# Optimization experiments

Measured on AMD Instinct MI355X. Metric: run time of the kernel, lower is better.

The kernel has to match this reference:

```python
import jax, jax.numpy as jnp
import numpy as np

B, H, W, C = 4, 448, 448, 3
P = 16
G = 28            # grid = H // P
T = G * G         # 784 patches
E = 768
HD = 3072
NH = 12
DH = E // NH
L = 6
LW = 9            # local_window


def _ln(x, g, b, eps=1e-5):
    m = x.mean(-1, keepdims=True)
    v = ((x - m) ** 2).mean(-1, keepdims=True)
    return (x - m) / jnp.sqrt(v + eps) * g + b


def _mask_bias():
    # torch bool attn_mask: True = disallowed. The module sets True for LOCAL
    # neighbors (|dr|<=lw//2 and |dc|<=lw//2), so local positions are MASKED OUT.
    idx = jnp.arange(T)
    r, c = idx // G, idx % G
    local = (jnp.abs(r[:, None] - r[None, :]) <= LW // 2) & \
            (jnp.abs(c[:, None] - c[None, :]) <= LW // 2)
    return jnp.where(local, -jnp.inf, 0.0).astype(jnp.float32)  # [T, T]


def _img_to_patch(x):
    # x: [B,H,W,C] -> [B,T,C*P*P], channel-major within a patch (matches torch code)
    x = x.transpose(0, 3, 1, 2)                       # [B,C,H,W]
    x = x.reshape(B, C, G, P, G, P)
    x = x.transpose(0, 2, 4, 1, 3, 5)                 # [B,G,G,C,P,P]
    return x.reshape(B, T, C * P * P)


def _forward(x, sxr_mean, sxr_std, input_w, input_b, pos_emb,
             ln1_w, ln1_b, in_w, in_b, out_w, out_b, ln2_w, ln2_b,
             w1, b1, w2, b2, head_ln_w, head_ln_b, head_w, head_b):
    h = _img_to_patch(x) @ input_w.T + input_b        # [B,T,E]
    h = (h.reshape(B, G, G, E) + pos_emb).reshape(B, T, E)
    bias = _mask_bias()

    def block(h, prm):
        l1w, l1b, iw, ib, ow, ob, l2w, l2b, W1, B1, W2, B2 = prm
        y = _ln(h, l1w, l1b)
        qkv = y @ iw.T + ib                           # [B,T,3E]
        q, k, v = jnp.split(qkv, 3, axis=-1)
        q = q.reshape(B, T, NH, DH)
        k = k.reshape(B, T, NH, DH)
        v = v.reshape(B, T, NH, DH)
        s = jnp.einsum('bqhd,bkhd->bhqk', q, k) / jnp.sqrt(jnp.float32(DH)) + bias
        a = jax.nn.softmax(s, axis=-1)
        o = jnp.einsum('bhqk,bkhd->bqhd', a, v).reshape(B, T, E)
        h = h + o @ ow.T + ob
        y2 = _ln(h, l2w, l2b)
        m = jax.nn.gelu(y2 @ W1.T + B1, approximate=False)  # torch nn.GELU default
        h = h + m @ W2.T + B2
        return h, None

    h, _ = jax.lax.scan(block, h, (ln1_w, ln1_b, in_w, in_b, out_w, out_b,
                                   ln2_w, ln2_b, w1, b1, w2, b2))

    logits = (_ln(h, head_ln_w, head_ln_b) @ head_w.T + head_b)[..., 0]  # [B,T]
    patch_flux = jnp.clip(10.0 ** (logits * sxr_std[0] + sxr_mean[0]) - 1e-8,
                          1e-15, 1.0)
    global_flux = jnp.maximum(patch_flux.sum(axis=1, keepdims=True), 1e-15)
    return global_flux, patch_flux


def setup_inputs() -> dict:
    key = jax.random.key(0)
    ks = iter(jax.random.split(key, 16))
    def p(shape, s=0.02):
        return jax.random.normal(next(ks), shape, jnp.float32) * s
    return dict(
        x=jax.random.normal(next(ks), (B, H, W, C), jnp.float32),
        sxr_mean=jnp.array([-6.0], jnp.float32),
        sxr_std=jnp.array([1.0], jnp.float32),
        input_w=p((E, C * P * P)), input_b=jnp.zeros(E, jnp.float32),
        pos_emb=p((1, G, G, E), 1.0),
        ln1_w=jnp.ones((L, E), jnp.float32), ln1_b=jnp.zeros((L, E), jnp.float32),
        in_w=p((L, 3 * E, E)), in_b=jnp.zeros((L, 3 * E), jnp.float32),
        out_w=p((L, E, E)), out_b=jnp.zeros((L, E), jnp.float32),
        ln2_w=jnp.ones((L, E), jnp.float32), ln2_b=jnp.zeros((L, E), jnp.float32),
        w1=p((L, HD, E)), b1=jnp.zeros((L, HD), jnp.float32),
        w2=p((L, E, HD)), b2=jnp.zeros((L, E), jnp.float32),
        head_ln_w=jnp.ones(E, jnp.float32), head_ln_b=jnp.zeros(E, jnp.float32),
        head_w=p((1, E)), head_b=jnp.zeros(1, jnp.float32),
    )


def reference(x, sxr_mean, sxr_std, input_w, input_b, pos_emb,
              ln1_w, ln1_b, in_w, in_b, out_w, out_b, ln2_w, ln2_b,
              w1, b1, w2, b2, head_ln_w, head_ln_b, head_w, head_b):
    return _forward(x, sxr_mean, sxr_std, input_w, input_b, pos_emb,
                    ln1_w, ln1_b, in_w, in_b, out_w, out_b, ln2_w, ln2_b,
                    w1, b1, w2, b2, head_ln_w, head_ln_b, head_w, head_b)
```

## Files before the change

### kernel.cpp

```cpp
#include <hip/hip_runtime.h>
#include <math.h>

#define BB 4
#define TT 784
#define GG 28
#define EE 768
#define HDIM 3072
#define NHEAD 12
#define NLAYER 6

typedef short bfrag __attribute__((ext_vector_type(8)));
typedef float ffrag __attribute__((ext_vector_type(4)));

__device__ __forceinline__ unsigned short f2b(float f) {
    union { float f; unsigned u; } v; v.f = f;
    unsigned r = v.u + 0x7FFF + ((v.u >> 16) & 1);
    return (unsigned short)(r >> 16);
}

#define GLOAD_LDS16(g, l)                                                          \
    __builtin_amdgcn_global_load_lds(                                              \
        (const __attribute__((address_space(1))) void*)(g),                        \
        (__attribute__((address_space(3))) void*)(l), 16, 0, 0)

__device__ __forceinline__ float block_reduce_sum256(float v, volatile float* sb) {
    #pragma unroll
    for (int m = 1; m < 64; m <<= 1) v += __shfl_xor(v, m, 64);
    int wave = threadIdx.x >> 6;
    if ((threadIdx.x & 63) == 0) sb[wave] = v;
    __syncthreads();
    return sb[0] + sb[1] + sb[2] + sb[3];
}

__global__ __launch_bounds__(256) void cast_kernel(const float* __restrict__ s,
                                                   unsigned short* __restrict__ d, int n4) {
    int i = blockIdx.x * 256 + threadIdx.x;
    if (i >= n4) return;
    float4 v = ((const float4*)s)[i];
    ushort4 o;
    o.x = f2b(v.x); o.y = f2b(v.y); o.z = f2b(v.z); o.w = f2b(v.w);
    ((ushort4*)d)[i] = o;
}

__global__ __launch_bounds__(256) void fused_cast_kernel(const float* __restrict__ iw,
                                                         const float* __restrict__ ow,
                                                         const float* __restrict__ W1,
                                                         const float* __restrict__ W2,
                                                         unsigned short* __restrict__ dq,
                                                         unsigned short* __restrict__ doo,
                                                         unsigned short* __restrict__ d1,
                                                         unsigned short* __restrict__ d2) {
    int i = blockIdx.x * 256 + threadIdx.x;
    const float* s; unsigned short* d; int k;
    if (i < 442368)            { s = iw;  d = dq;  k = i; }
    else if (i < 589824)       { s = ow;  d = doo; k = i - 442368; }
    else if (i < 1179648)      { s = W1;  d = d1;  k = i - 589824; }
    else if (i < 1769472)      { s = W2;  d = d2;  k = i - 1179648; }
    else return;
    float4 v = ((const float4*)s)[k];
    ushort4 o;
    o.x = f2b(v.x); o.y = f2b(v.y); o.z = f2b(v.z); o.w = f2b(v.w);
    ((ushort4*)d)[k] = o;
}

__global__ __launch_bounds__(256) void patchify_kernel(const float* __restrict__ x,
                                                       unsigned short* __restrict__ P) {
    int idx = blockIdx.x * blockDim.x + threadIdx.x;
    const int total = BB * TT * EE;
    if (idx >= total) return;
    int k = idx % EE;
    int t = (idx / EE) % TT;
    int b = idx / (EE * TT);
    int c = k >> 8;
    int rem = k & 255;
    int p1 = rem >> 4;
    int p2 = rem & 15;
    int g1 = t / GG, g2 = t % GG;
    int hh = g1 * 16 + p1, ww = g2 * 16 + p2;
    P[idx] = f2b(x[((b * 448 + hh) * 448 + ww) * 3 + c]);
}

__global__ __launch_bounds__(256) void posfill_kernel(float* __restrict__ h,
                                                      const float* __restrict__ pos) {
    int idx = blockIdx.x * blockDim.x + threadIdx.x;
    const int total = BB * TT * EE;
    if (idx >= total) return;
    h[idx] = pos[idx % (TT * EE)];
}

__global__ __launch_bounds__(256) void ln_kernel(const float* __restrict__ X,
                                                 const float* __restrict__ g,
                                                 const float* __restrict__ bt,
                                                 unsigned short* __restrict__ Yb,
                                                 float* Yf) {
    __shared__ float sb1[4];
    __shared__ float sb2[4];
    int row = blockIdx.x;
    int tid = threadIdx.x;
    const float* x = X + (size_t)row * EE;
    float v0 = x[tid], v1 = x[tid + 256], v2 = x[tid + 512];
    float s = block_reduce_sum256(v0 + v1 + v2, sb1);
    float mean = s * (1.0f / 768.0f);
    float d0 = v0 - mean, d1 = v1 - mean, d2 = v2 - mean;
    __syncthreads();
    float ss = block_reduce_sum256(d0 * d0 + d1 * d1 + d2 * d2, sb2);
    float rstd = rsqrtf(ss * (1.0f / 768.0f) + 1e-5f);
    float y0 = d0 * rstd * g[tid]       + bt[tid];
    float y1 = d1 * rstd * g[tid + 256] + bt[tid + 256];
    float y2 = d2 * rstd * g[tid + 512] + bt[tid + 512];
    unsigned short* yb = Yb + (size_t)row * EE;
    yb[tid] = f2b(y0); yb[tid + 256] = f2b(y1); yb[tid + 512] = f2b(y2);
    if (Yf) {
        float* yf = Yf + (size_t)row * EE;
        yf[tid] = y0; yf[tid + 256] = y1; yf[tid + 512] = y2;
    }
}

__global__ __launch_bounds__(256) void gemm_bf16(const unsigned short* __restrict__ A,
                                                 const unsigned short* __restrict__ W,
                                                 const float* __restrict__ bias,
                                                 const float* R, float* C,
                                                 unsigned short* Cb,
                                                 int M, int N, int K, int act) {
    __shared__ unsigned short As[128 * 32];
    __shared__ unsigned short Ws[128 * 32];
    int tid = threadIdx.x;
    int wave = tid >> 6, lane = tid & 63;
    int m0 = blockIdx.y << 7, n0 = blockIdx.x << 7;
    int mh = (wave & 1) << 6, nh = (wave >> 1) << 6;

    int cl = lane & 15, qd = lane >> 4;
    int sr = lane >> 2;
    int sc = (lane & 3) << 3;

    const unsigned short* Ap[2];
    const unsigned short* Wp[2];
    unsigned short* lA[2];
    unsigned short* lW[2];
    #pragma unroll
    for (int i = 0; i < 2; i++) {
        int ar = m0 + (wave << 5) + (i << 4) + sr;
        if (ar > M - 1) ar = M - 1;
        Ap[i] = A + (size_t)ar * K + sc;
        int wr = n0 + (wave << 5) + (i << 4) + sr;
        Wp[i] = W + (size_t)wr * K + sc;
        lA[i] = &As[((wave << 5) + (i << 4)) << 5];
        lW[i] = &Ws[((wave << 5) + (i << 4)) << 5];
    }

    ffrag acc[4][4] = {};

    for (int k0 = 0; k0 < K; k0 += 32) {
        __syncthreads();
        GLOAD_LDS16(Ap[0] + k0, lA[0]);
        GLOAD_LDS16(Ap[1] + k0, lA[1]);
        GLOAD_LDS16(Wp[0] + k0, lW[0]);
        GLOAD_LDS16(Wp[1] + k0, lW[1]);
        __syncthreads();

        bfrag af[4], bfr[4];
        #pragma unroll
        for (int i = 0; i < 4; i++)
            af[i] = *(const bfrag*)&As[(((mh + (i << 4) + cl)) << 5) + (qd << 3)];
        #pragma unroll
        for (int j = 0; j < 4; j++)
            bfr[j] = *(const bfrag*)&Ws[(((nh + (j << 4) + cl)) << 5) + (qd << 3)];
        #pragma unroll
        for (int i = 0; i < 4; i++)
            #pragma unroll
            for (int j = 0; j < 4; j++)
                acc[i][j] = __builtin_amdgcn_mfma_f32_16x16x32_bf16(af[i], bfr[j], acc[i][j], 0, 0, 0);
    }

    #pragma unroll
    for (int j = 0; j < 4; j++) {
        int col = n0 + nh + (j << 4) + cl;
        float bv = bias[col];
        #pragma unroll
        for (int i = 0; i < 4; i++) {
            int row0 = m0 + mh + (i << 4) + (qd << 2);
            #pragma unroll
            for (int r = 0; r < 4; r++) {
                int row = row0 + r;
                if (row < M) {
                    float v = acc[i][j][r] + bv;
                    if (R) v += R[(size_t)row * N + col];
                    if (act) v = 0.5f * v * (1.0f + erff(v * 0.70710678118654752f));
                    if (C)  C[(size_t)row * N + col] = v;
                    if (Cb) Cb[(size_t)row * N + col] = f2b(v);
                }
            }
        }
    }
}

__global__ __launch_bounds__(256) void gemm_bf16_sk(const unsigned short* __restrict__ A,
                                                    const unsigned short* __restrict__ W,
                                                    const float* __restrict__ bias,
                                                    float* C,
                                                    int M, int N, int K, int KC) {
    __shared__ unsigned short As[128 * 32];
    __shared__ unsigned short Ws[128 * 32];
    int tid = threadIdx.x;
    int wave = tid >> 6, lane = tid & 63;
    int m0 = blockIdx.y << 7, n0 = blockIdx.x << 7;
    int mh = (wave & 1) << 6, nh = (wave >> 1) << 6;
    int z = blockIdx.z;
    int kbeg = z * KC;
    int kend = kbeg + KC > K ? K : kbeg + KC;

    int cl = lane & 15, qd = lane >> 4;
    int sr = lane >> 2;
    int sc = (lane & 3) << 3;

    const unsigned short* Ap[2];
    const unsigned short* Wp[2];
    unsigned short* lA[2];
    unsigned short* lW[2];
    #pragma unroll
    for (int i = 0; i < 2; i++) {
        int ar = m0 + (wave << 5) + (i << 4) + sr;
        if (ar > M - 1) ar = M - 1;
        Ap[i] = A + (size_t)ar * K + sc;
        int wr = n0 + (wave << 5) + (i << 4) + sr;
        Wp[i] = W + (size_t)wr * K + sc;
        lA[i] = &As[((wave << 5) + (i << 4)) << 5];
        lW[i] = &Ws[((wave << 5) + (i << 4)) << 5];
    }

    ffrag acc[4][4] = {};

    for (int k0 = kbeg; k0 < kend; k0 += 32) {
        __syncthreads();
        GLOAD_LDS16(Ap[0] + k0, lA[0]);
        GLOAD_LDS16(Ap[1] + k0, lA[1]);
        GLOAD_LDS16(Wp[0] + k0, lW[0]);
        GLOAD_LDS16(Wp[1] + k0, lW[1]);
        __syncthreads();

        bfrag af[4], bfr[4];
        #pragma unroll
        for (int i = 0; i < 4; i++)
            af[i] = *(const bfrag*)&As[(((mh + (i << 4) + cl)) << 5) + (qd << 3)];
        #pragma unroll
        for (int j = 0; j < 4; j++)
            bfr[j] = *(const bfrag*)&Ws[(((nh + (j << 4) + cl)) << 5) + (qd << 3)];
        #pragma unroll
        for (int i = 0; i < 4; i++)
            #pragma unroll
            for (int j = 0; j < 4; j++)
                acc[i][j] = __builtin_amdgcn_mfma_f32_16x16x32_bf16(af[i], bfr[j], acc[i][j], 0, 0, 0);
    }

    #pragma unroll
    for (int j = 0; j < 4; j++) {
        int col = n0 + nh + (j << 4) + cl;
        float bv = (z == 0) ? bias[col] : 0.0f;
        #pragma unroll
        for (int i = 0; i < 4; i++) {
            int row0 = m0 + mh + (i << 4) + (qd << 2);
            #pragma unroll
            for (int r = 0; r < 4; r++) {
                int row = row0 + r;
                if (row < M)
                    unsafeAtomicAdd(&C[(size_t)row * N + col], acc[i][j][r] + bv);
            }
        }
    }
}

#define APAD 72
__global__ __launch_bounds__(256) void attn_kernel(const unsigned short* __restrict__ qkv,
                                                   unsigned short* __restrict__ O) {
    __shared__ unsigned short Ks[64 * APAD];
    __shared__ unsigned short Vt[64 * APAD];
    __shared__ unsigned short Pb[64 * APAD];
    int tid = threadIdx.x;
    int wave = tid >> 6, lane = tid & 63;
    int cl = lane & 15, qd = lane >> 4;
    int bh = blockIdx.y;
    int b = bh / NHEAD, hh = bh % NHEAD;
    int q0 = blockIdx.x * 64;

    int qrow = q0 + wave * 16 + cl;
    if (qrow > TT - 1) qrow = TT - 1;
    const unsigned short* qbase = qkv + (size_t)(b * TT + qrow) * 2304 + hh * 64;
    bfrag qf0 = *(const bfrag*)(qbase + (qd << 3));
    bfrag qf1 = *(const bfrag*)(qbase + 32 + (qd << 3));

    ffrag o_acc[4] = {};
    float m_run[4], l_run[4];
    int qg_[4], qr_[4], qc_[4];
    #pragma unroll
    for (int r = 0; r < 4; r++) {
        qg_[r] = q0 + wave * 16 + (qd << 2) + r;
        qr_[r] = qg_[r] / GG;
        qc_[r] = qg_[r] % GG;
        m_run[r] = -1e30f; l_run[r] = 0.0f;
    }

    int srow = tid >> 3;
    int sd = (tid & 7) << 3;

    for (int k0 = 0; k0 < 832; k0 += 64) {
        __syncthreads();
        #pragma unroll
        for (int it = 0; it < 2; it++) {
            int row = it * 32 + srow;
            int kg = k0 + row;
            int kgc = kg > TT - 1 ? TT - 1 : kg;
            const unsigned short* kb = qkv + (size_t)(b * TT + kgc) * 2304 + 768 + hh * 64 + sd;
            bfrag kv = *(const bfrag*)kb;
            *(bfrag*)&Ks[row * APAD + sd] = kv;
            bfrag vv = *(const bfrag*)(kb + 768);
            #pragma unroll
            for (int j = 0; j < 8; j++)
                Vt[(sd + j) * APAD + row] = vv[j];
        }
        __syncthreads();

        ffrag s[4];
        #pragma unroll
        for (int j = 0; j < 4; j++) {
            ffrag z = {0.f, 0.f, 0.f, 0.f};
            bfrag kf0 = *(const bfrag*)&Ks[(j * 16 + cl) * APAD + (qd << 3)];
            bfrag kf1 = *(const bfrag*)&Ks[(j * 16 + cl) * APAD + 32 + (qd << 3)];
            z = __builtin_amdgcn_mfma_f32_16x16x32_bf16(qf0, kf0, z, 0, 0, 0);
            z = __builtin_amdgcn_mfma_f32_16x16x32_bf16(qf1, kf1, z, 0, 0, 0);
            s[j] = z;
        }

        #pragma unroll
        for (int j = 0; j < 4; j++) {
            int kg = k0 + j * 16 + cl;
            int kr = kg / GG, kc = kg % GG;
            #pragma unroll
            for (int r = 0; r < 4; r++) {
                bool masked = (kg >= TT) ||
                              (abs(qr_[r] - kr) <= 4 && abs(qc_[r] - kc) <= 4);
                s[j][r] = masked ? -3.0e38f : s[j][r] * 0.125f;
            }
        }

        float p_[4][4];
        #pragma unroll
        for (int r = 0; r < 4; r++) {
            float mx = fmaxf(fmaxf(s[0][r], s[1][r]), fmaxf(s[2][r], s[3][r]));
            mx = fmaxf(mx, __shfl_xor(mx, 1, 64));
            mx = fmaxf(mx, __shfl_xor(mx, 2, 64));
            mx = fmaxf(mx, __shfl_xor(mx, 4, 64));
            mx = fmaxf(mx, __shfl_xor(mx, 8, 64));
            float m_new = fmaxf(m_run[r], mx);
            float alpha = __expf(m_run[r] - m_new);
            float rs = 0.f;
            #pragma unroll
            for (int j = 0; j < 4; j++) {
                float pv = __expf(s[j][r] - m_new);
                p_[j][r] = pv;
                rs += pv;
            }
            rs += __shfl_xor(rs, 1, 64);
            rs += __shfl_xor(rs, 2, 64);
            rs += __shfl_xor(rs, 4, 64);
            rs += __shfl_xor(rs, 8, 64);
            l_run[r] = l_run[r] * alpha + rs;
            m_run[r] = m_new;
            #pragma unroll
            for (int t = 0; t < 4; t++) o_acc[t][r] *= alpha;
        }

        #pragma unroll
        for (int j = 0; j < 4; j++)
            #pragma unroll
            for (int r = 0; r < 4; r++)
                Pb[(wave * 16 + (qd << 2) + r) * APAD + j * 16 + cl] = f2b(p_[j][r]);
        __syncthreads();

        bfrag pf0 = *(const bfrag*)&Pb[(wave * 16 + cl) * APAD + (qd << 3)];
        bfrag pf1 = *(const bfrag*)&Pb[(wave * 16 + cl) * APAD + 32 + (qd << 3)];
        #pragma unroll
        for (int t = 0; t < 4; t++) {
            bfrag vf0 = *(const bfrag*)&Vt[(t * 16 + cl) * APAD + (qd << 3)];
            bfrag vf1 = *(const bfrag*)&Vt[(t * 16 + cl) * APAD + 32 + (qd << 3)];
            o_acc[t] = __builtin_amdgcn_mfma_f32_16x16x32_bf16(pf0, vf0, o_acc[t], 0, 0, 0);
            o_acc[t] = __builtin_amdgcn_mfma_f32_16x16x32_bf16(pf1, vf1, o_acc[t], 0, 0, 0);
        }
    }

    #pragma unroll
    for (int r = 0; r < 4; r++) {
        if (qg_[r] < TT) {
            float inv = 1.0f / fmaxf(l_run[r], 1e-30f);
            #pragma unroll
            for (int t = 0; t < 4; t++)
                O[(size_t)(b * TT + qg_[r]) * EE + hh * 64 + t * 16 + cl] =
                    f2b(o_acc[t][r] * inv);
        }
    }
}

__global__ __launch_bounds__(256) void head_kernel(const float* __restrict__ Y,
                                                   const float* __restrict__ hw,
                                                   const float* __restrict__ hb,
                                                   const float* __restrict__ mean_,
                                                   const float* __restrict__ std_,
                                                   float* __restrict__ out) {
    __shared__ float sb[4];
    int row = blockIdx.x;
    int tid = threadIdx.x;
    const float* y = Y + (size_t)row * EE;
    float v = y[tid] * hw[tid] + y[tid + 256] * hw[tid + 256] + y[tid + 512] * hw[tid + 512];
    v = block_reduce_sum256(v, sb);
    if (tid == 0) {
        float logit = v + hb[0];
        float z = logit * std_[0] + mean_[0];
        float f = expf(z * 2.302585092994046f) - 1e-8f;
        f = fminf(fmaxf(f, 1e-15f), 1.0f);
        out[4 + row] = f;
    }
}

__global__ __launch_bounds__(256) void flux_sum_kernel(float* __restrict__ out) {
    __shared__ float sb[4];
    int b = blockIdx.x;
    int tid = threadIdx.x;
    const float* pf = out + 4 + (size_t)b * TT;
    float v = pf[tid] + pf[tid + 256] + pf[tid + 512];
    if (tid < TT - 768) v += pf[tid + 768];
    v = block_reduce_sum256(v, sb);
    if (tid == 0) out[b] = fmaxf(v, 1e-15f);
}

extern "C" void kernel_launch(void* const* d_in, const int* in_sizes, int n_in,
                              void* d_out, int out_size, void* d_ws, size_t ws_size,
                              hipStream_t stream) {
    const float* x        = (const float*)d_in[0];
    const float* sxr_mean = (const float*)d_in[1];
    const float* sxr_std  = (const float*)d_in[2];
    const float* input_w  = (const float*)d_in[3];
    const float* input_b  = (const float*)d_in[4];
    const float* pos_emb  = (const float*)d_in[5];
    const float* ln1_w    = (const float*)d_in[6];
    const float* ln1_b    = (const float*)d_in[7];
    const float* in_w     = (const float*)d_in[8];
    const float* in_b     = (const float*)d_in[9];
    const float* out_w    = (const float*)d_in[10];
    const float* out_b    = (const float*)d_in[11];
    const float* ln2_w    = (const float*)d_in[12];
    const float* ln2_b    = (const float*)d_in[13];
    const float* w1       = (const float*)d_in[14];
    const float* b1       = (const float*)d_in[15];
    const float* w2       = (const float*)d_in[16];
    const float* b2       = (const float*)d_in[17];
    const float* head_ln_w = (const float*)d_in[18];
    const float* head_ln_b = (const float*)d_in[19];
    const float* head_w   = (const float*)d_in[20];
    const float* head_b   = (const float*)d_in[21];
    float* out = (float*)d_out;

    const size_t NROW = (size_t)BB * TT;
    const size_t NE   = NROW * EE;

    float* h   = (float*)d_ws;
    float* y32 = h + NE;
    unsigned short* qkv_b = (unsigned short*)(y32 + NE);
    unsigned short* y_b   = qkv_b + NROW * 3 * EE;
    unsigned short* o_b   = y_b + NE;
    unsigned short* mlp_b = o_b + NE;
    unsigned short* wq_b  = mlp_b + NROW * HDIM;
    unsigned short* wo_b  = wq_b + (size_t)3 * EE * EE;
    unsigned short* w1_b  = wo_b + (size_t)EE * EE;
    unsigned short* w2_b  = w1_b + (size_t)HDIM * EE;

    const int tot = BB * TT * EE;
    const int GY = (int)((NROW + 127) / 128);

    patchify_kernel<<<(tot + 255) / 256, 256, 0, stream>>>(x, mlp_b);
    cast_kernel<<<(EE * EE / 4 + 255) / 256, 256, 0, stream>>>(input_w, wo_b, EE * EE / 4);
    posfill_kernel<<<(tot + 255) / 256, 256, 0, stream>>>(h, pos_emb);
    gemm_bf16_sk<<<dim3(EE / 128, GY, 2), 256, 0, stream>>>(
        mlp_b, wo_b, input_b, h, (int)NROW, EE, EE, 384);

    for (int l = 0; l < NLAYER; l++) {
        fused_cast_kernel<<<6912, 256, 0, stream>>>(
            in_w + (size_t)l * 3 * EE * EE, out_w + (size_t)l * EE * EE,
            w1 + (size_t)l * HDIM * EE, w2 + (size_t)l * EE * HDIM,
            wq_b, wo_b, w1_b, w2_b);

        ln_kernel<<<(int)NROW, 256, 0, stream>>>(h, ln1_w + l * EE, ln1_b + l * EE, y_b, nullptr);
        gemm_bf16<<<dim3(3 * EE / 128, GY), 256, 0, stream>>>(
            y_b, wq_b, in_b + (size_t)l * 3 * EE, nullptr, nullptr, qkv_b,
            (int)NROW, 3 * EE, EE, 0);
        attn_kernel<<<dim3(13, BB * NHEAD), 256, 0, stream>>>(qkv_b, o_b);
        gemm_bf16_sk<<<dim3(EE / 128, GY, 2), 256, 0, stream>>>(
            o_b, wo_b, out_b + (size_t)l * EE, h, (int)NROW, EE, EE, 384);
        ln_kernel<<<(int)NROW, 256, 0, stream>>>(h, ln2_w + l * EE, ln2_b + l * EE, y_b, nullptr);
        gemm_bf16<<<dim3(HDIM / 128, GY), 256, 0, stream>>>(
            y_b, w1_b, b1 + (size_t)l * HDIM, nullptr, nullptr, mlp_b,
            (int)NROW, HDIM, EE, 1);
        gemm_bf16_sk<<<dim3(EE / 128, GY, 4), 256, 0, stream>>>(
            mlp_b, w2_b, b2 + (size_t)l * EE, h, (int)NROW, EE, HDIM, 768);
    }

    ln_kernel<<<(int)NROW, 256, 0, stream>>>(h, head_ln_w, head_ln_b, y_b, y32);
    head_kernel<<<(int)NROW, 256, 0, stream>>>(y32, head_w, head_b, sxr_mean, sxr_std, out);
    flux_sum_kernel<<<BB, 256, 0, stream>>>(out);
}
```

Measured before the change: 1.753 ms.

## Split QKV output into Q, K and pre-transposed V; widen attention query tiles

The QKV GEMM now writes Q and K to separate buffers and V to a per-head transposed, token-padded buffer. This lets the attention kernel load V tiles with vector copies instead of scalar transposes into shared memory. The attention kernel handles 128 queries per block, two 16-row subtiles per wave, so each K/V tile is reused across more queries. It also folds the softmax scale into exp2, updates mask coordinates incrementally, and replaces a block barrier with a wave-local LDS wait. The cost is more registers per thread and a scattered transposed-V store in the GEMM epilogue. The padded V columns past the last token are never written, so the result depends on that memory holding finite values, since their zero probabilities are still multiplied in.

```diff
diff --git a/kernel.cpp b/kernel.cpp
--- a/kernel.cpp
+++ b/kernel.cpp
@@ -8,6 +8,7 @@
 #define HDIM 3072
 #define NHEAD 12
 #define NLAYER 6
+#define TTP 832
 
 typedef short bfrag __attribute__((ext_vector_type(8)));
 typedef float ffrag __attribute__((ext_vector_type(4)));
@@ -194,6 +195,106 @@
     }
 }
 
+__global__ __launch_bounds__(256) void gemm_qkv(const unsigned short* __restrict__ A,
+                                                const unsigned short* __restrict__ W,
+                                                const float* __restrict__ bias,
+                                                unsigned short* __restrict__ Q,
+                                                unsigned short* __restrict__ Kd,
+                                                unsigned short* __restrict__ vT,
+                                                int M, int N, int K) {
+    __shared__ unsigned short As[128 * 32];
+    __shared__ unsigned short Ws[128 * 32];
+    int tid = threadIdx.x;
+    int wave = tid >> 6, lane = tid & 63;
+    int m0 = blockIdx.y << 7, n0 = blockIdx.x << 7;
+    int mh = (wave & 1) << 6, nh = (wave >> 1) << 6;
+
+    int cl = lane & 15, qd = lane >> 4;
+    int sr = lane >> 2;
+    int sc = (lane & 3) << 3;
+
+    const unsigned short* Ap[2];
+    const unsigned short* Wp[2];
+    unsigned short* lA[2];
+    unsigned short* lW[2];
+    #pragma unroll
+    for (int i = 0; i < 2; i++) {
+        int ar = m0 + (wave << 5) + (i << 4) + sr;
+        if (ar > M - 1) ar = M - 1;
+        Ap[i] = A + (size_t)ar * K + sc;
+        int wr = n0 + (wave << 5) + (i << 4) + sr;
+        Wp[i] = W + (size_t)wr * K + sc;
+        lA[i] = &As[((wave << 5) + (i << 4)) << 5];
+        lW[i] = &Ws[((wave << 5) + (i << 4)) << 5];
+    }
+
+    ffrag acc[4][4] = {};
+
+    for (int k0 = 0; k0 < K; k0 += 32) {
+        __syncthreads();
+        GLOAD_LDS16(Ap[0] + k0, lA[0]);
+        GLOAD_LDS16(Ap[1] + k0, lA[1]);
+        GLOAD_LDS16(Wp[0] + k0, lW[0]);
+        GLOAD_LDS16(Wp[1] + k0, lW[1]);
+        __syncthreads();
+
+        bfrag af[4], bfr[4];
+        #pragma unroll
+        for (int i = 0; i < 4; i++)
+            af[i] = *(const bfrag*)&As[(((mh + (i << 4) + cl)) << 5) + (qd << 3)];
+        #pragma unroll
+        for (int j = 0; j < 4; j++)
+            bfr[j] = *(const bfrag*)&Ws[(((nh + (j << 4) + cl)) << 5) + (qd << 3)];
+        #pragma unroll
+        for (int i = 0; i < 4; i++)
+            #pragma unroll
+            for (int j = 0; j < 4; j++)
+                acc[i][j] = __builtin_amdgcn_mfma_f32_16x16x32_bf16(af[i], bfr[j], acc[i][j], 0, 0, 0);
+    }
+
+    int nb = n0 + nh;
+    if (nb < 1536) {
+        unsigned short* dst = (nb < 768) ? Q : Kd;
+        int cb = (nb < 768) ? 0 : 768;
+        #pragma unroll
+        for (int j = 0; j < 4; j++) {
+            int col = nb + (j << 4) + cl;
+            float bv = bias[col];
+            #pragma unroll
+            for (int i = 0; i < 4; i++) {
+                int row0 = m0 + mh + (i << 4) + (qd << 2);
+                #pragma unroll
+                for (int r = 0; r < 4; r++) {
+                    int row = row0 + r;
+                    if (row < M)
+                        dst[(size_t)row * EE + col - cb] = f2b(acc[i][j][r] + bv);
+                }
+            }
+        }
+    } else {
+        int hh = (nb - 1536) >> 6;
+        #pragma unroll
+        for (int i = 0; i < 4; i++) {
+            int row0 = m0 + mh + (i << 4) + (qd << 2);
+            #pragma unroll
+            for (int r = 0; r < 4; r++) {
+                int row = row0 + r;
+                if (row < M) {
+                    int b = row / TT;
+                    int t = row - b * TT;
+                    size_t vbase = ((size_t)(b * NHEAD + hh) * 64) * TTP + t;
+                    #pragma unroll
+                    for (int j = 0; j < 4; j++) {
+                        int col = nb + (j << 4) + cl;
+                        vT[vbase + (size_t)((j << 4) + cl) * TTP] =
+                            f2b(acc[i][j][r] + bias[col]);
+                    }
+                }
+            }
+        }
+    }
+}
+
 __global__ __launch_bounds__(256) void gemm_bf16_sk(const unsigned short* __restrict__ A,
                                                     const unsigned short* __restrict__ W,
                                                     const float* __restrict__ bias,
@@ -269,134 +370,165 @@
     }
 }
 
-#define APAD 72
-__global__ __launch_bounds__(256) void attn_kernel(const unsigned short* __restrict__ qkv,
+#define LP 72
+#define SCL2 0.18033688011112042f
+__global__ __launch_bounds__(256) void attn_kernel(const unsigned short* __restrict__ Qg,
+                                                   const unsigned short* __restrict__ Kg,
+                                                   const unsigned short* __restrict__ vT,
                                                    unsigned short* __restrict__ O) {
-    __shared__ unsigned short Ks[64 * APAD];
-    __shared__ unsigned short Vt[64 * APAD];
-    __shared__ unsigned short Pb[64 * APAD];
+    __shared__ unsigned short Ks[64 * LP];
+    __shared__ unsigned short Vt[64 * LP];
+    __shared__ unsigned short Pb[128 * LP];
     int tid = threadIdx.x;
     int wave = tid >> 6, lane = tid & 63;
     int cl = lane & 15, qd = lane >> 4;
     int bh = blockIdx.y;
     int b = bh / NHEAD, hh = bh % NHEAD;
-    int q0 = blockIdx.x * 64;
-
-    int qrow = q0 + wave * 16 + cl;
-    if (qrow > TT - 1) qrow = TT - 1;
-    const unsigned short* qbase = qkv + (size_t)(b * TT + qrow) * 2304 + hh * 64;
-    bfrag qf0 = *(const bfrag*)(qbase + (qd << 3));
-    bfrag qf1 = *(const bfrag*)(qbase + 32 + (qd << 3));
-
-    ffrag o_acc[4] = {};
-    float m_run[4], l_run[4];
-    int qg_[4], qr_[4], qc_[4];
-    #pragma unroll
-    for (int r = 0; r < 4; r++) {
-        qg_[r] = q0 + wave * 16 + (qd << 2) + r;
-        qr_[r] = qg_[r] / GG;
-        qc_[r] = qg_[r] % GG;
-        m_run[r] = -1e30f; l_run[r] = 0.0f;
-    }
-
+    int q0 = blockIdx.x * 128;
+    int qw = q0 + wave * 32;
+
+    bfrag qf[2][2];
+    #pragma unroll
+    for (int s = 0; s < 2; s++) {
+        int qrow = qw + s * 16 + cl;
+        if (qrow > TT - 1) qrow = TT - 1;
+        const unsigned short* qb = Qg + (size_t)(b * TT + qrow) * EE + hh * 64;
+        qf[s][0] = *(const bfrag*)(qb + (qd << 3));
+        qf[s][1] = *(const bfrag*)(qb + 32 + (qd << 3));
+    }
+
+    ffrag o_acc[2][4] = {};
+    float m_run[2][4], l_run[2][4];
+    int qg_[2][4], qr_[2][4], qc_[2][4];
+    #pragma unroll
+    for (int s = 0; s < 2; s++)
+        #pragma unroll
+        for (int r = 0; r < 4; r++) {
+            qg_[s][r] = qw + s * 16 + (qd << 2) + r;
+            qr_[s][r] = qg_[s][r] / GG;
+            qc_[s][r] = qg_[s][r] % GG;
+            m_run[s][r] = -1e30f; l_run[s][r] = 0.0f;
+        }
+
+    int kr[4], kc[4];
+    #pragma unroll
+    for (int j = 0; j < 4; j++) {
+        int kg = j * 16 + cl;
+        kr[j] = kg / GG; kc[j] = kg % GG;
+    }
+
+    const unsigned short* kbase = Kg + (size_t)b * TT * EE + hh * 64;
+    const unsigned short* vbase = vT + (size_t)(b * NHEAD + hh) * 64 * TTP;
     int srow = tid >> 3;
-    int sd = (tid & 7) << 3;
+    int scol = (tid & 7) << 3;
 
     for (int k0 = 0; k0 < 832; k0 += 64) {
         __syncthreads();
         #pragma unroll
         for (int it = 0; it < 2; it++) {
             int row = it * 32 + srow;
-            int kg = k0 + row;
-            int kgc = kg > TT - 1 ? TT - 1 : kg;
-            const unsigned short* kb = qkv + (size_t)(b * TT + kgc) * 2304 + 768 + hh * 64 + sd;
-            bfrag kv = *(const bfrag*)kb;
-            *(bfrag*)&Ks[row * APAD + sd] = kv;
-            bfrag vv = *(const bfrag*)(kb + 768);
-            #pragma unroll
-            for (int j = 0; j < 8; j++)
-                Vt[(sd + j) * APAD + row] = vv[j];
-        }
-        __syncthreads();
-
-        ffrag s[4];
+            int tok = k0 + row; if (tok > TT - 1) tok = TT - 1;
+            *(bfrag*)&Ks[row * LP + scol] =
+                *(const bfrag*)(kbase + (size_t)tok * EE + scol);
+            *(bfrag*)&Vt[row * LP + scol] =
+                *(const bfrag*)(vbase + (size_t)row * TTP + k0 + scol);
+        }
+        __syncthreads();
+
+        ffrag sv[2][4];
         #pragma unroll
         for (int j = 0; j < 4; j++) {
-            ffrag z = {0.f, 0.f, 0.f, 0.f};
-            bfrag kf0 = *(const bfrag*)&Ks[(j * 16 + cl) * APAD + (qd << 3)];
-            bfrag kf1 = *(const bfrag*)&Ks[(j * 16 + cl) * APAD + 32 + (qd << 3)];
-            z = __builtin_amdgcn_mfma_f32_16x16x32_bf16(qf0, kf0, z, 0, 0, 0);
-            z = __builtin_amdgcn_mfma_f32_16x16x32_bf16(qf1, kf1, z, 0, 0, 0);
-            s[j] = z;
+            bfrag kf0 = *(const bfrag*)&Ks[(j * 16 + cl) * LP + (qd << 3)];
+            bfrag kf1 = *(const bfrag*)&Ks[(j * 16 + cl) * LP + 32 + (qd << 3)];
+            #pragma unroll
+            for (int s = 0; s < 2; s++) {
+                ffrag z = {0.f, 0.f, 0.f, 0.f};
+                z = __builtin_amdgcn_mfma_f32_16x16x32_bf16(qf[s][0], kf0, z, 0, 0, 0);
+                z = __builtin_amdgcn_mfma_f32_16x16x32_bf16(qf[s][1], kf1, z, 0, 0, 0);
+                sv[s][j] = z;
+            }
+        }
+
+        #pragma unroll
+        for (int s = 0; s < 2; s++) {
+            #pragma unroll
+            for (int j = 0; j < 4; j++) {
+                #pragma unroll
+                for (int r = 0; r < 4; r++) {
+                    bool masked = (kr[j] > 27) ||
+                                  (abs(qr_[s][r] - kr[j]) <= 4 && abs(qc_[s][r] - kc[j]) <= 4);
+                    if (masked) sv[s][j][r] = -3.0e38f;
+                }
+            }
+            #pragma unroll
+            for (int r = 0; r < 4; r++) {
+                float mx = fmaxf(fmaxf(sv[s][0][r], sv[s][1][r]),
+                                 fmaxf(sv[s][2][r], sv[s][3][r]));
+                mx = fmaxf(mx, __shfl_xor(mx, 1, 64));
+                mx = fmaxf(mx, __shfl_xor(mx, 2, 64));
+                mx = fmaxf(mx, __shfl_xor(mx, 4, 64));
+                mx = fmaxf(mx, __shfl_xor(mx, 8, 64));
+                float m_new = fmaxf(m_run[s][r], mx);
+                float alpha = exp2f((m_run[s][r] - m_new) * SCL2);
+                float rs = 0.f;
+                float p0 = exp2f((sv[s][0][r] - m_new) * SCL2);
+                float p1 = exp2f((sv[s][1][r] - m_new) * SCL2);
+                float p2 = exp2f((sv[s][2][r] - m_new) * SCL2);
+                float p3 = exp2f((sv[s][3][r] - m_new) * SCL2);
+                rs = (p0 + p1) + (p2 + p3);
+                rs += __shfl_xor(rs, 1, 64);
+                rs += __shfl_xor(rs, 2, 64);
+                rs += __shfl_xor(rs, 4, 64);
+                rs += __shfl_xor(rs, 8, 64);
+                l_run[s][r] = l_run[s][r] * alpha + rs;
+                m_run[s][r] = m_new;
+                #pragma unroll
+                for (int t = 0; t < 4; t++) o_acc[s][t][r] *= alpha;
+                int prow = (wave * 32 + s * 16 + (qd << 2) + r) * LP;
+                Pb[prow + 0 * 16 + cl] = f2b(p0);
+                Pb[prow + 1 * 16 + cl] = f2b(p1);
+                Pb[prow + 2 * 16 + cl] = f2b(p2);
+                Pb[prow + 3 * 16 + cl] = f2b(p3);
+            }
+        }
+        asm volatile("s_waitcnt lgkmcnt(0)" ::: "memory");
+
+        bfrag pf[2][2];
+        #pragma unroll
+        for (int s = 0; s < 2; s++) {
+            pf[s][0] = *(const bfrag*)&Pb[(wave * 32 + s * 16 + cl) * LP + (qd << 3)];
+            pf[s][1] = *(const bfrag*)&Pb[(wave * 32 + s * 16 + cl) * LP + 32 + (qd << 3)];
+        }
+        #pragma unroll
+        for (int t = 0; t < 4; t++) {
+            bfrag vf0 = *(const bfrag*)&Vt[(t * 16 + cl) * LP + (qd << 3)];
+            bfrag vf1 = *(const bfrag*)&Vt[(t * 16 + cl) * LP + 32 + (qd << 3)];
+            #pragma unroll
+            for (int s = 0; s < 2; s++) {
+                o_acc[s][t] = __builtin_amdgcn_mfma_f32_16x16x32_bf16(pf[s][0], vf0, o_acc[s][t], 0, 0, 0);
+                o_acc[s][t] = __builtin_amdgcn_mfma_f32_16x16x32_bf16(pf[s][1], vf1, o_acc[s][t], 0, 0, 0);
+            }
         }
 
         #pragma unroll
         for (int j = 0; j < 4; j++) {
-            int kg = k0 + j * 16 + cl;
-            int kr = kg / GG, kc = kg % GG;
-            #pragma unroll
-            for (int r = 0; r < 4; r++) {
-                bool masked = (kg >= TT) ||
-                              (abs(qr_[r] - kr) <= 4 && abs(qc_[r] - kc) <= 4);
-                s[j][r] = masked ? -3.0e38f : s[j][r] * 0.125f;
-            }
-        }
-
-        float p_[4][4];
+            kc[j] += 8; kr[j] += 2;
+            if (kc[j] >= GG) { kc[j] -= GG; kr[j] += 1; }
+        }
+    }
+
+    #pragma unroll
+    for (int s = 0; s < 2; s++)
         #pragma unroll
         for (int r = 0; r < 4; r++) {
-            float mx = fmaxf(fmaxf(s[0][r], s[1][r]), fmaxf(s[2][r], s[3][r]));
-            mx = fmaxf(mx, __shfl_xor(mx, 1, 64));
-            mx = fmaxf(mx, __shfl_xor(mx, 2, 64));
-            mx = fmaxf(mx, __shfl_xor(mx, 4, 64));
-            mx = fmaxf(mx, __shfl_xor(mx, 8, 64));
-            float m_new = fmaxf(m_run[r], mx);
-            float alpha = __expf(m_run[r] - m_new);
-            float rs = 0.f;
-            #pragma unroll
-            for (int j = 0; j < 4; j++) {
-                float pv = __expf(s[j][r] - m_new);
-                p_[j][r] = pv;
-                rs += pv;
-            }
-            rs += __shfl_xor(rs, 1, 64);
-            rs += __shfl_xor(rs, 2, 64);
-            rs += __shfl_xor(rs, 4, 64);
-            rs += __shfl_xor(rs, 8, 64);
-            l_run[r] = l_run[r] * alpha + rs;
-            m_run[r] = m_new;
-            #pragma unroll
-            for (int t = 0; t < 4; t++) o_acc[t][r] *= alpha;
-        }
-
-        #pragma unroll
-        for (int j = 0; j < 4; j++)
-            #pragma unroll
-            for (int r = 0; r < 4; r++)
-                Pb[(wave * 16 + (qd << 2) + r) * APAD + j * 16 + cl] = f2b(p_[j][r]);
-        __syncthreads();
-
-        bfrag pf0 = *(const bfrag*)&Pb[(wave * 16 + cl) * APAD + (qd << 3)];
-        bfrag pf1 = *(const bfrag*)&Pb[(wave * 16 + cl) * APAD + 32 + (qd << 3)];
-        #pragma unroll
-        for (int t = 0; t < 4; t++) {
-            bfrag vf0 = *(const bfrag*)&Vt[(t * 16 + cl) * APAD + (qd << 3)];
-            bfrag vf1 = *(const bfrag*)&Vt[(t * 16 + cl) * APAD + 32 + (qd << 3)];
-            o_acc[t] = __builtin_amdgcn_mfma_f32_16x16x32_bf16(pf0, vf0, o_acc[t], 0, 0, 0);
-            o_acc[t] = __builtin_amdgcn_mfma_f32_16x16x32_bf16(pf1, vf1, o_acc[t], 0, 0, 0);
-        }
-    }
-
-    #pragma unroll
-    for (int r = 0; r < 4; r++) {
-        if (qg_[r] < TT) {
-            float inv = 1.0f / fmaxf(l_run[r], 1e-30f);
-            #pragma unroll
-            for (int t = 0; t < 4; t++)
-                O[(size_t)(b * TT + qg_[r]) * EE + hh * 64 + t * 16 + cl] =
-                    f2b(o_acc[t][r] * inv);
-        }
-    }
+            if (qg_[s][r] < TT) {
+                float inv = 1.0f / fmaxf(l_run[s][r], 1e-30f);
+                #pragma unroll
+                for (int t = 0; t < 4; t++)
+                    O[(size_t)(b * TT + qg_[s][r]) * EE + hh * 64 + t * 16 + cl] =
+                        f2b(o_acc[s][t][r] * inv);
+            }
+        }
 }
 
 __global__ __launch_bounds__(256) void head_kernel(const float* __restrict__ Y,
@@ -463,8 +595,10 @@
 
     float* h   = (float*)d_ws;
     float* y32 = h + NE;
-    unsigned short* qkv_b = (unsigned short*)(y32 + NE);
-    unsigned short* y_b   = qkv_b + NROW * 3 * EE;
+    unsigned short* q_b   = (unsigned short*)(y32 + NE);
+    unsigned short* k_b   = q_b + NE;
+    unsigned short* vT_b  = k_b + NE;
+    unsigned short* y_b   = vT_b + (size_t)BB * NHEAD * 64 * TTP;
     unsigned short* o_b   = y_b + NE;
     unsigned short* mlp_b = o_b + NE;
     unsigned short* wq_b  = mlp_b + NROW * HDIM;
@@ -488,10 +622,10 @@
             wq_b, wo_b, w1_b, w2_b);
 
         ln_kernel<<<(int)NROW, 256, 0, stream>>>(h, ln1_w + l * EE, ln1_b + l * EE, y_b, nullptr);
-        gemm_bf16<<<dim3(3 * EE / 128, GY), 256, 0, stream>>>(
-            y_b, wq_b, in_b + (size_t)l * 3 * EE, nullptr, nullptr, qkv_b,
-            (int)NROW, 3 * EE, EE, 0);
-        attn_kernel<<<dim3(13, BB * NHEAD), 256, 0, stream>>>(qkv_b, o_b);
+        gemm_qkv<<<dim3(3 * EE / 128, GY), 256, 0, stream>>>(
+            y_b, wq_b, in_b + (size_t)l * 3 * EE, q_b, k_b, vT_b,
+            (int)NROW, 3 * EE, EE);
+        attn_kernel<<<dim3(7, BB * NHEAD), 256, 0, stream>>>(q_b, k_b, vT_b, o_b);
         gemm_bf16_sk<<<dim3(EE / 128, GY, 2), 256, 0, stream>>>(
             o_b, wo_b, out_b + (size_t)l * EE, h, (int)NROW, EE, EE, 384);
         ln_kernel<<<(int)NROW, 256, 0, stream>>>(h, ln2_w + l * EE, ln2_b + l * EE, y_b, nullptr);
```

Result: slower. 1.926 ms (+9.9%).
